# Kernel optimization log

Measured on AMD Instinct MI355X. Metric: run time of the kernel, lower is better.

The kernel has to match this reference:

```python
import jax, jax.numpy as jnp
import numpy as np

B, C, H, W = 16, 64, 128, 128
E = 8          # number of experts
TOPK = 2       # num_expert (top-k routing)


def setup_inputs() -> dict:
    key = jax.random.key(0)
    ks = jax.random.split(key, 8)
    s = 1.0 / np.sqrt(C)
    x = jax.random.normal(ks[0], (B, C, H, W), dtype=jnp.float32)
    k = jax.random.normal(ks[1], (B, C, 1, 1), dtype=jnp.float32)
    Wg = jax.random.normal(ks[2], (C, E), dtype=jnp.float32) * s
    bg = jnp.zeros((E,), dtype=jnp.float32)
    W1 = jax.random.normal(ks[3], (E, C, C), dtype=jnp.float32) * s  # [E, out, in]
    b1 = jnp.zeros((E, C), dtype=jnp.float32)
    W2 = jax.random.normal(ks[4], (E, C, C), dtype=jnp.float32) * s
    b2 = jnp.zeros((E, C), dtype=jnp.float32)
    return {"x": x, "k": k, "Wg": Wg, "bg": bg, "W1": W1, "b1": b1, "W2": W2, "b2": b2}


def reference(x, k, Wg, bg, W1, b1, W2, b2):
    # --- gate: global avg pool + linear -> [B, E] logits ---
    pooled = x.mean(axis=(2, 3))                              # [B, C]
    logits = pooled @ Wg + bg                                  # [B, E]
    # softmax in fp32 then cast back (matches F.softmax(dtype=torch.float).to(x.dtype))
    weights = jax.nn.softmax(logits.astype(jnp.float32), axis=1).astype(x.dtype)
    topk_w, topk_idx = jax.lax.top_k(weights, TOPK)           # [B, TOPK]
    # scatter top-k weights into dense per-expert mask [B, E]
    mask = jnp.zeros_like(weights).at[jnp.arange(B)[:, None], topk_idx].set(topk_w)
    # --- training branch: run ALL experts, combine with mask ---
    # expert_e(x, k) = W2_e @ gelu((W1_e @ x + b1_e) * k) + b2_e   (1x1 convs)
    h = jnp.einsum('eoc,bchw->ebohw', W1, x) + b1[:, None, :, None, None]
    h = jax.nn.gelu(h * k[None])                               # [E, B, C, H, W]
    y = jnp.einsum('eoc,ebchw->ebohw', W2, h) + b2[:, None, :, None, None]
    out = x + jnp.einsum('ebchw,be->bchw', y, mask)
    return out
```

## Files before the change

### kernel.cpp

```cpp
#include <hip/hip_runtime.h>
#include <hip/hip_bf16.h>


#define BB 16
#define CC 64
#define EE 8
#define HWPX 16384
#define LSTR 40

typedef __bf16 bf16x8 __attribute__((ext_vector_type(8)));
typedef float f32x4 __attribute__((ext_vector_type(4)));

__device__ __forceinline__ unsigned packbf2(float lo, float hi) {
    __bf16 a = (__bf16)lo, b = (__bf16)hi;
    unsigned short ua = __builtin_bit_cast(unsigned short, a);
    unsigned short ub = __builtin_bit_cast(unsigned short, b);
    return ((unsigned)ub << 16) | (unsigned)ua;
}

__global__ __launch_bounds__(256) void pool_conv_kernel(
    const float* __restrict__ x, float* __restrict__ pooled,
    const float* __restrict__ W1, const float* __restrict__ W2,
    __bf16* __restrict__ W1b, __bf16* __restrict__ W2b) {
    int blk = blockIdx.x;
    if (blk < BB * CC) {
        const float4* p = (const float4*)(x + (size_t)blk * HWPX);
        float s = 0.f;
        for (int i = threadIdx.x; i < HWPX / 4; i += 256) {
            float4 v = p[i];
            s += (v.x + v.y) + (v.z + v.w);
        }
        #pragma unroll
        for (int off = 32; off > 0; off >>= 1) s += __shfl_down(s, off);
        __shared__ float ls[4];
        if ((threadIdx.x & 63) == 0) ls[threadIdx.x >> 6] = s;
        __syncthreads();
        if (threadIdx.x == 0) pooled[blk] = ((ls[0] + ls[1]) + (ls[2] + ls[3])) * (1.0f / (float)HWPX);
    } else {
        int i = (blk - BB * CC) * 256 + threadIdx.x;
        W1b[i] = (__bf16)W1[i];
        W2b[i] = (__bf16)W2[i];
    }
}

__global__ void gate_kernel(const float* __restrict__ pooled,
                            const float* __restrict__ Wg,
                            const float* __restrict__ bg,
                            int* __restrict__ gidx, float* __restrict__ gw) {
    int b = threadIdx.x;
    if (b >= BB) return;
    float logits[EE];
    #pragma unroll
    for (int e = 0; e < EE; ++e) logits[e] = bg[e];
    for (int c = 0; c < CC; ++c) {
        float pv = pooled[b * CC + c];
        #pragma unroll
        for (int e = 0; e < EE; ++e) logits[e] = fmaf(pv, Wg[c * EE + e], logits[e]);
    }
    float m = logits[0];
    #pragma unroll
    for (int e = 1; e < EE; ++e) m = fmaxf(m, logits[e]);
    float w[EE]; float den = 0.f;
    #pragma unroll
    for (int e = 0; e < EE; ++e) { w[e] = expf(logits[e] - m); den += w[e]; }
    float inv = 1.0f / den;
    #pragma unroll
    for (int e = 0; e < EE; ++e) w[e] *= inv;
    int i0 = 0;
    #pragma unroll
    for (int e = 1; e < EE; ++e) if (w[e] > w[i0]) i0 = e;
    int i1 = -1;
    #pragma unroll
    for (int e = 0; e < EE; ++e) {
        if (e == i0) continue;
        if (i1 < 0 || w[e] > w[i1]) i1 = e;
    }
    gidx[b * 2 + 0] = i0; gidx[b * 2 + 1] = i1;
    gw[b * 2 + 0] = w[i0]; gw[b * 2 + 1] = w[i1];
}

__global__ __launch_bounds__(256) void moe_main(
    const float* __restrict__ x, const float* __restrict__ kvec,
    const __bf16* __restrict__ W1b, const float* __restrict__ b1,
    const __bf16* __restrict__ W2b, const float* __restrict__ b2,
    const int* __restrict__ gidx, const float* __restrict__ gw,
    float* __restrict__ out) {

    __shared__ unsigned int xT32[64 * LSTR];
    __shared__ unsigned int hT32[2][64 * LSTR];

    const int blk = blockIdx.x;
    const int b = blk >> 8;
    const int p0 = (blk & 255) << 6;
    const int t = threadIdx.x;
    const int w = t >> 6;
    const int l = t & 63;
    const int g = l >> 4;
    const int l15 = l & 15;

    const int arow = 16 * w + l15;
    const int r0w = 16 * w + 4 * g;

    const int e0 = __builtin_amdgcn_readfirstlane(gidx[b * 2 + 0]);
    const int e1 = __builtin_amdgcn_readfirstlane(gidx[b * 2 + 1]);
    const float wgt0 = gw[b * 2 + 0];
    const float wgt1 = gw[b * 2 + 1];

    bf16x8 a1f[2][2], a2f[2][2];
    #pragma unroll
    for (int ks = 0; ks < 2; ++ks) {
        a1f[0][ks] = *(const bf16x8*)(W1b + e0 * CC * CC + arow * CC + ks * 32 + g * 8);
        a1f[1][ks] = *(const bf16x8*)(W1b + e1 * CC * CC + arow * CC + ks * 32 + g * 8);
        a2f[0][ks] = *(const bf16x8*)(W2b + e0 * CC * CC + arow * CC + ks * 32 + g * 8);
        a2f[1][ks] = *(const bf16x8*)(W2b + e1 * CC * CC + arow * CC + ks * 32 + g * 8);
    }
    float b1j[2][4], b2j[2][4], kkj[4];
    #pragma unroll
    for (int j = 0; j < 4; ++j) {
        b1j[0][j] = b1[e0 * CC + r0w + j];
        b1j[1][j] = b1[e1 * CC + r0w + j];
        b2j[0][j] = b2[e0 * CC + r0w + j];
        b2j[1][j] = b2[e1 * CC + r0w + j];
        kkj[j]    = kvec[b * CC + r0w + j];
    }

    {
        const int c0 = (t & 31) * 2;
        const int px0 = (t >> 5) * 8;
        const float* r0 = x + ((size_t)(b * CC + c0)) * HWPX + p0 + px0;
        const float* r1 = r0 + HWPX;
        float4 A0 = *(const float4*)(r0);
        float4 A1 = *(const float4*)(r0 + 4);
        float4 B0 = *(const float4*)(r1);
        float4 B1 = *(const float4*)(r1 + 4);
        float av[8] = {A0.x, A0.y, A0.z, A0.w, A1.x, A1.y, A1.z, A1.w};
        float bv[8] = {B0.x, B0.y, B0.z, B0.w, B1.x, B1.y, B1.z, B1.w};
        #pragma unroll
        for (int i = 0; i < 8; ++i)
            xT32[(px0 + i) * LSTR + (t & 31)] = packbf2(av[i], bv[i]);
    }
    __syncthreads();

    bf16x8 bx[4][2];
    #pragma unroll
    for (int cb = 0; cb < 4; ++cb)
        #pragma unroll
        for (int ks = 0; ks < 2; ++ks)
            bx[cb][ks] = *(const bf16x8*)&xT32[(cb * 16 + l15) * LSTR + ks * 16 + g * 4];

    f32x4 acc2[4];
    #pragma unroll
    for (int cb = 0; cb < 4; ++cb) acc2[cb] = (f32x4){0.f, 0.f, 0.f, 0.f};

    const float C1 = -2.302208239f;
    const float C2 = -0.1029434f;

    #pragma unroll
    for (int s = 0; s < 2; ++s) {
        const float wgt = s ? wgt1 : wgt0;

        f32x4 hacc[4];
        #pragma unroll
        for (int cb = 0; cb < 4; ++cb) {
            hacc[cb] = (f32x4){0.f, 0.f, 0.f, 0.f};
            #pragma unroll
            for (int ks = 0; ks < 2; ++ks)
                hacc[cb] = __builtin_amdgcn_mfma_f32_16x16x32_bf16(a1f[s][ks], bx[cb][ks], hacc[cb], 0, 0, 0);
        }

        #pragma unroll
        for (int cb = 0; cb < 4; ++cb) {
            float hv[4];
            #pragma unroll
            for (int j = 0; j < 4; ++j) {
                float a = hacc[cb][j] + b1j[s][j];
                float tt = a * kkj[j];
                float tt2 = tt * tt;
                float arg = tt * fmaf(C2, tt2, C1);
                float ex = __builtin_amdgcn_exp2f(arg);
                float r = __builtin_amdgcn_rcpf(ex + 1.f);
                hv[j] = (tt * wgt) * r;
            }
            const int px = cb * 16 + l15;
            uint2 pk;
            pk.x = packbf2(hv[0], hv[1]);
            pk.y = packbf2(hv[2], hv[3]);
            *(uint2*)&hT32[s][px * LSTR + 8 * w + 2 * g] = pk;
        }
        __syncthreads();

        #pragma unroll
        for (int cb = 0; cb < 4; ++cb) {
            #pragma unroll
            for (int ks = 0; ks < 2; ++ks) {
                bf16x8 bh = *(const bf16x8*)&hT32[s][(cb * 16 + l15) * LSTR + ks * 16 + g * 4];
                acc2[cb] = __builtin_amdgcn_mfma_f32_16x16x32_bf16(a2f[s][ks], bh, acc2[cb], 0, 0, 0);
            }
        }

        #pragma unroll
        for (int j = 0; j < 4; ++j) {
            float bb = wgt * b2j[s][j];
            #pragma unroll
            for (int cb = 0; cb < 4; ++cb) acc2[cb][j] += bb;
        }
    }

    const float* xbase = x + (size_t)b * CC * HWPX + p0;
    float* obase = out + (size_t)b * CC * HWPX + p0;
    #pragma unroll
    for (int cb = 0; cb < 4; ++cb) {
        const int col = cb * 16 + l15;
        #pragma unroll
        for (int j = 0; j < 4; ++j) {
            size_t off = (size_t)(r0w + j) * HWPX + col;
            __builtin_nontemporal_store(xbase[off] + acc2[cb][j], &obase[off]);
        }
    }
}

extern "C" void kernel_launch(void* const* d_in, const int* in_sizes, int n_in,
                              void* d_out, int out_size, void* d_ws, size_t ws_size,
                              hipStream_t stream) {
    const float* x  = (const float*)d_in[0];
    const float* k  = (const float*)d_in[1];
    const float* Wg = (const float*)d_in[2];
    const float* bg = (const float*)d_in[3];
    const float* W1 = (const float*)d_in[4];
    const float* b1 = (const float*)d_in[5];
    const float* W2 = (const float*)d_in[6];
    const float* b2 = (const float*)d_in[7];
    float* out = (float*)d_out;

    float*  pooled = (float*)d_ws;
    int*    gidx   = (int*)((char*)d_ws + 4096);
    float*  gw     = (float*)((char*)d_ws + 4096 + 128);
    __bf16* W1b    = (__bf16*)((char*)d_ws + 8192);
    __bf16* W2b    = (__bf16*)((char*)d_ws + 8192 + 65536);

    pool_conv_kernel<<<BB * CC + EE * CC * CC / 256, 256, 0, stream>>>(x, pooled, W1, W2, W1b, W2b);
    gate_kernel<<<1, 64, 0, stream>>>(pooled, Wg, bg, gidx, gw);
    moe_main<<<BB * 256, 256, 0, stream>>>(x, k, W1b, b1, W2b, b2, gidx, gw, out);
}
```

Baseline: 57.33 us.

## Restructure MoE main kernel: swizzled LDS reuse, interleaved expert GEMMs, early residual loads

Replaces the padded LDS layout with an XOR-swizzled 32-word stride and reuses the x buffer for the second expert's hidden tile, cutting LDS footprint from three buffers to two. Both experts' first GEMMs and GELUs are interleaved for more ILP. W2 fragment loads and residual x loads are deferred and issued ahead of the second GEMM to overlap with LDS work. The bias terms are folded into one combined sum, and the output uses normal rather than nontemporal stores. The interleaving and early loads raise register pressure.

Result: no change. 56.57 us (-1.3%).

```diff
diff --git a/kernel.cpp b/kernel.cpp
--- a/kernel.cpp
+++ b/kernel.cpp
@@ -6,7 +6,6 @@
 #define CC 64
 #define EE 8
 #define HWPX 16384
-#define LSTR 40
 
 typedef __bf16 bf16x8 __attribute__((ext_vector_type(8)));
 typedef float f32x4 __attribute__((ext_vector_type(4)));
@@ -16,6 +15,10 @@
     unsigned short ua = __builtin_bit_cast(unsigned short, a);
     unsigned short ub = __builtin_bit_cast(unsigned short, b);
     return ((unsigned)ub << 16) | (unsigned)ua;
+}
+
+__device__ __forceinline__ int swz(int px, int d) {
+    return px * 32 + ((d & ~3) ^ ((px & 7) << 2)) + (d & 3);
 }
 
 __global__ __launch_bounds__(256) void pool_conv_kernel(
@@ -86,8 +89,7 @@
     const int* __restrict__ gidx, const float* __restrict__ gw,
     float* __restrict__ out) {
 
-    __shared__ unsigned int xT32[64 * LSTR];
-    __shared__ unsigned int hT32[2][64 * LSTR];
+    __shared__ unsigned int lds[2][64 * 32];
 
     const int blk = blockIdx.x;
     const int b = blk >> 8;
@@ -106,13 +108,11 @@
     const float wgt0 = gw[b * 2 + 0];
     const float wgt1 = gw[b * 2 + 1];
 
-    bf16x8 a1f[2][2], a2f[2][2];
+    bf16x8 a1f[2][2];
     #pragma unroll
     for (int ks = 0; ks < 2; ++ks) {
         a1f[0][ks] = *(const bf16x8*)(W1b + e0 * CC * CC + arow * CC + ks * 32 + g * 8);
         a1f[1][ks] = *(const bf16x8*)(W1b + e1 * CC * CC + arow * CC + ks * 32 + g * 8);
-        a2f[0][ks] = *(const bf16x8*)(W2b + e0 * CC * CC + arow * CC + ks * 32 + g * 8);
-        a2f[1][ks] = *(const bf16x8*)(W2b + e1 * CC * CC + arow * CC + ks * 32 + g * 8);
     }
     float b1j[2][4], b2j[2][4], kkj[4];
     #pragma unroll
@@ -125,9 +125,9 @@
     }
 
     {
-        const int c0 = (t & 31) * 2;
+        const int c0 = (t & 31);
         const int px0 = (t >> 5) * 8;
-        const float* r0 = x + ((size_t)(b * CC + c0)) * HWPX + p0 + px0;
+        const float* r0 = x + ((size_t)(b * CC + c0 * 2)) * HWPX + p0 + px0;
         const float* r1 = r0 + HWPX;
         float4 A0 = *(const float4*)(r0);
         float4 A1 = *(const float4*)(r0 + 4);
@@ -137,7 +137,7 @@
         float bv[8] = {B0.x, B0.y, B0.z, B0.w, B1.x, B1.y, B1.z, B1.w};
         #pragma unroll
         for (int i = 0; i < 8; ++i)
-            xT32[(px0 + i) * LSTR + (t & 31)] = packbf2(av[i], bv[i]);
+            lds[0][swz(px0 + i, c0)] = packbf2(av[i], bv[i]);
     }
     __syncthreads();
 
@@ -146,67 +146,98 @@
     for (int cb = 0; cb < 4; ++cb)
         #pragma unroll
         for (int ks = 0; ks < 2; ++ks)
-            bx[cb][ks] = *(const bf16x8*)&xT32[(cb * 16 + l15) * LSTR + ks * 16 + g * 4];
-
-    f32x4 acc2[4];
-    #pragma unroll
-    for (int cb = 0; cb < 4; ++cb) acc2[cb] = (f32x4){0.f, 0.f, 0.f, 0.f};
+            bx[cb][ks] = *(const bf16x8*)&lds[0][swz(cb * 16 + l15, ks * 16 + g * 4)];
 
     const float C1 = -2.302208239f;
     const float C2 = -0.1029434f;
 
-    #pragma unroll
-    for (int s = 0; s < 2; ++s) {
-        const float wgt = s ? wgt1 : wgt0;
-
-        f32x4 hacc[4];
-        #pragma unroll
-        for (int cb = 0; cb < 4; ++cb) {
-            hacc[cb] = (f32x4){0.f, 0.f, 0.f, 0.f};
-            #pragma unroll
-            for (int ks = 0; ks < 2; ++ks)
-                hacc[cb] = __builtin_amdgcn_mfma_f32_16x16x32_bf16(a1f[s][ks], bx[cb][ks], hacc[cb], 0, 0, 0);
-        }
-
-        #pragma unroll
-        for (int cb = 0; cb < 4; ++cb) {
-            float hv[4];
-            #pragma unroll
-            for (int j = 0; j < 4; ++j) {
-                float a = hacc[cb][j] + b1j[s][j];
-                float tt = a * kkj[j];
-                float tt2 = tt * tt;
-                float arg = tt * fmaf(C2, tt2, C1);
-                float ex = __builtin_amdgcn_exp2f(arg);
-                float r = __builtin_amdgcn_rcpf(ex + 1.f);
-                hv[j] = (tt * wgt) * r;
-            }
-            const int px = cb * 16 + l15;
-            uint2 pk;
-            pk.x = packbf2(hv[0], hv[1]);
-            pk.y = packbf2(hv[2], hv[3]);
-            *(uint2*)&hT32[s][px * LSTR + 8 * w + 2 * g] = pk;
-        }
-        __syncthreads();
-
-        #pragma unroll
-        for (int cb = 0; cb < 4; ++cb) {
-            #pragma unroll
-            for (int ks = 0; ks < 2; ++ks) {
-                bf16x8 bh = *(const bf16x8*)&hT32[s][(cb * 16 + l15) * LSTR + ks * 16 + g * 4];
-                acc2[cb] = __builtin_amdgcn_mfma_f32_16x16x32_bf16(a2f[s][ks], bh, acc2[cb], 0, 0, 0);
-            }
-        }
-
+    f32x4 h0[4], h1[4];
+    #pragma unroll
+    for (int cb = 0; cb < 4; ++cb) {
+        h0[cb] = (f32x4){0.f, 0.f, 0.f, 0.f};
+        h1[cb] = (f32x4){0.f, 0.f, 0.f, 0.f};
+        #pragma unroll
+        for (int ks = 0; ks < 2; ++ks) {
+            h0[cb] = __builtin_amdgcn_mfma_f32_16x16x32_bf16(a1f[0][ks], bx[cb][ks], h0[cb], 0, 0, 0);
+            h1[cb] = __builtin_amdgcn_mfma_f32_16x16x32_bf16(a1f[1][ks], bx[cb][ks], h1[cb], 0, 0, 0);
+        }
+    }
+
+    uint2 p0k[4], p1k[4];
+    #pragma unroll
+    for (int cb = 0; cb < 4; ++cb) {
+        float hv0[4], hv1[4];
         #pragma unroll
         for (int j = 0; j < 4; ++j) {
-            float bb = wgt * b2j[s][j];
-            #pragma unroll
-            for (int cb = 0; cb < 4; ++cb) acc2[cb][j] += bb;
-        }
-    }
+            float a0 = h0[cb][j] + b1j[0][j];
+            float t0 = a0 * kkj[j];
+            float ex0 = __builtin_amdgcn_exp2f(t0 * fmaf(C2, t0 * t0, C1));
+            hv0[j] = (t0 * wgt0) * __builtin_amdgcn_rcpf(ex0 + 1.f);
+            float a1 = h1[cb][j] + b1j[1][j];
+            float t1 = a1 * kkj[j];
+            float ex1 = __builtin_amdgcn_exp2f(t1 * fmaf(C2, t1 * t1, C1));
+            hv1[j] = (t1 * wgt1) * __builtin_amdgcn_rcpf(ex1 + 1.f);
+        }
+        p0k[cb].x = packbf2(hv0[0], hv0[1]);
+        p0k[cb].y = packbf2(hv0[2], hv0[3]);
+        p1k[cb].x = packbf2(hv1[0], hv1[1]);
+        p1k[cb].y = packbf2(hv1[2], hv1[3]);
+    }
+
+    #pragma unroll
+    for (int cb = 0; cb < 4; ++cb)
+        *(uint2*)&lds[1][swz(cb * 16 + l15, 8 * w + 2 * g)] = p0k[cb];
+
+    bf16x8 a2f[2][2];
+    #pragma unroll
+    for (int ks = 0; ks < 2; ++ks) {
+        a2f[0][ks] = *(const bf16x8*)(W2b + e0 * CC * CC + arow * CC + ks * 32 + g * 8);
+        a2f[1][ks] = *(const bf16x8*)(W2b + e1 * CC * CC + arow * CC + ks * 32 + g * 8);
+    }
+
+    __syncthreads();
+
+    #pragma unroll
+    for (int cb = 0; cb < 4; ++cb)
+        *(uint2*)&lds[0][swz(cb * 16 + l15, 8 * w + 2 * g)] = p1k[cb];
 
     const float* xbase = x + (size_t)b * CC * HWPX + p0;
+    float xp[4][4];
+    #pragma unroll
+    for (int cb = 0; cb < 4; ++cb)
+        #pragma unroll
+        for (int j = 0; j < 4; ++j)
+            xp[cb][j] = xbase[(size_t)(r0w + j) * HWPX + cb * 16 + l15];
+
+    f32x4 acc2[4];
+    #pragma unroll
+    for (int cb = 0; cb < 4; ++cb) acc2[cb] = (f32x4){0.f, 0.f, 0.f, 0.f};
+
+    #pragma unroll
+    for (int cb = 0; cb < 4; ++cb) {
+        #pragma unroll
+        for (int ks = 0; ks < 2; ++ks) {
+            bf16x8 bh = *(const bf16x8*)&lds[1][swz(cb * 16 + l15, ks * 16 + g * 4)];
+            acc2[cb] = __builtin_amdgcn_mfma_f32_16x16x32_bf16(a2f[0][ks], bh, acc2[cb], 0, 0, 0);
+        }
+    }
+
+    __syncthreads();
+
+    #pragma unroll
+    for (int cb = 0; cb < 4; ++cb) {
+        #pragma unroll
+        for (int ks = 0; ks < 2; ++ks) {
+            bf16x8 bh = *(const bf16x8*)&lds[0][swz(cb * 16 + l15, ks * 16 + g * 4)];
+            acc2[cb] = __builtin_amdgcn_mfma_f32_16x16x32_bf16(a2f[1][ks], bh, acc2[cb], 0, 0, 0);
+        }
+    }
+
+    float bsum[4];
+    #pragma unroll
+    for (int j = 0; j < 4; ++j)
+        bsum[j] = fmaf(wgt0, b2j[0][j], wgt1 * b2j[1][j]);
+
     float* obase = out + (size_t)b * CC * HWPX + p0;
     #pragma unroll
     for (int cb = 0; cb < 4; ++cb) {
@@ -214,7 +245,7 @@
         #pragma unroll
         for (int j = 0; j < 4; ++j) {
             size_t off = (size_t)(r0w + j) * HWPX + col;
-            __builtin_nontemporal_store(xbase[off] + acc2[cb][j], &obase[off]);
+            obase[off] = xp[cb][j] + (acc2[cb][j] + bsum[j]);
         }
     }
 }
```

## Give each wave its own pixel tile so x is reused from registers

Applied to the files above, without the earlier changes.

Each wave now owns 16 pixels and computes all 64 output channels across four row tiles, instead of the block sharing a transposed x tile and splitting channels across waves. The x values are loaded once into registers and reused for the residual add, which removes the second global read of x. Per-wave swizzled LDS buffers replace the block-wide padded buffers and __syncthreads barriers. The b2 bias terms are pre-combined. In exchange, every wave now loads the full weight matrices, which adds register pressure under the launch_bounds(256,4) hint, and x loads are only 16 pixels wide per channel row and uses plain rather than nontemporal stores.

Result: slower. 95.80 us (+67.1%).

```diff
diff --git a/kernel.cpp b/kernel.cpp
--- a/kernel.cpp
+++ b/kernel.cpp
@@ -6,7 +6,6 @@
 #define CC 64
 #define EE 8
 #define HWPX 16384
-#define LSTR 40
 
 typedef __bf16 bf16x8 __attribute__((ext_vector_type(8)));
 typedef float f32x4 __attribute__((ext_vector_type(4)));
@@ -16,6 +15,10 @@
     unsigned short ua = __builtin_bit_cast(unsigned short, a);
     unsigned short ub = __builtin_bit_cast(unsigned short, b);
     return ((unsigned)ub << 16) | (unsigned)ua;
+}
+
+__device__ __forceinline__ int swz16(int p, int d) {
+    return p * 32 + ((d & ~3) ^ ((p & 7) << 2)) + (d & 3);
 }
 
 __global__ __launch_bounds__(256) void pool_conv_kernel(
@@ -79,144 +82,160 @@
     gw[b * 2 + 0] = w[i0]; gw[b * 2 + 1] = w[i1];
 }
 
-__global__ __launch_bounds__(256) void moe_main(
+__global__ __launch_bounds__(256, 4) void moe_main(
     const float* __restrict__ x, const float* __restrict__ kvec,
     const __bf16* __restrict__ W1b, const float* __restrict__ b1,
     const __bf16* __restrict__ W2b, const float* __restrict__ b2,
     const int* __restrict__ gidx, const float* __restrict__ gw,
     float* __restrict__ out) {
 
-    __shared__ unsigned int xT32[64 * LSTR];
-    __shared__ unsigned int hT32[2][64 * LSTR];
+    __shared__ unsigned int LH[4][2][16 * 32];
 
     const int blk = blockIdx.x;
     const int b = blk >> 8;
-    const int p0 = (blk & 255) << 6;
+    const int P0 = (blk & 255) << 6;
     const int t = threadIdx.x;
     const int w = t >> 6;
     const int l = t & 63;
     const int g = l >> 4;
     const int l15 = l & 15;
-
-    const int arow = 16 * w + l15;
-    const int r0w = 16 * w + 4 * g;
+    const int px = P0 + 16 * w + l15;
 
     const int e0 = __builtin_amdgcn_readfirstlane(gidx[b * 2 + 0]);
     const int e1 = __builtin_amdgcn_readfirstlane(gidx[b * 2 + 1]);
     const float wgt0 = gw[b * 2 + 0];
     const float wgt1 = gw[b * 2 + 1];
 
-    bf16x8 a1f[2][2], a2f[2][2];
-    #pragma unroll
-    for (int ks = 0; ks < 2; ++ks) {
-        a1f[0][ks] = *(const bf16x8*)(W1b + e0 * CC * CC + arow * CC + ks * 32 + g * 8);
-        a1f[1][ks] = *(const bf16x8*)(W1b + e1 * CC * CC + arow * CC + ks * 32 + g * 8);
-        a2f[0][ks] = *(const bf16x8*)(W2b + e0 * CC * CC + arow * CC + ks * 32 + g * 8);
-        a2f[1][ks] = *(const bf16x8*)(W2b + e1 * CC * CC + arow * CC + ks * 32 + g * 8);
-    }
-    float b1j[2][4], b2j[2][4], kkj[4];
-    #pragma unroll
-    for (int j = 0; j < 4; ++j) {
-        b1j[0][j] = b1[e0 * CC + r0w + j];
-        b1j[1][j] = b1[e1 * CC + r0w + j];
-        b2j[0][j] = b2[e0 * CC + r0w + j];
-        b2j[1][j] = b2[e1 * CC + r0w + j];
-        kkj[j]    = kvec[b * CC + r0w + j];
-    }
-
-    {
-        const int c0 = (t & 31) * 2;
-        const int px0 = (t >> 5) * 8;
-        const float* r0 = x + ((size_t)(b * CC + c0)) * HWPX + p0 + px0;
-        const float* r1 = r0 + HWPX;
-        float4 A0 = *(const float4*)(r0);
-        float4 A1 = *(const float4*)(r0 + 4);
-        float4 B0 = *(const float4*)(r1);
-        float4 B1 = *(const float4*)(r1 + 4);
-        float av[8] = {A0.x, A0.y, A0.z, A0.w, A1.x, A1.y, A1.z, A1.w};
-        float bv[8] = {B0.x, B0.y, B0.z, B0.w, B1.x, B1.y, B1.z, B1.w};
-        #pragma unroll
-        for (int i = 0; i < 8; ++i)
-            xT32[(px0 + i) * LSTR + (t & 31)] = packbf2(av[i], bv[i]);
-    }
-    __syncthreads();
-
-    bf16x8 bx[4][2];
-    #pragma unroll
-    for (int cb = 0; cb < 4; ++cb)
-        #pragma unroll
-        for (int ks = 0; ks < 2; ++ks)
-            bx[cb][ks] = *(const bf16x8*)&xT32[(cb * 16 + l15) * LSTR + ks * 16 + g * 4];
-
-    f32x4 acc2[4];
-    #pragma unroll
-    for (int cb = 0; cb < 4; ++cb) acc2[cb] = (f32x4){0.f, 0.f, 0.f, 0.f};
+    const float* xb = x + b * CC * HWPX + px;
+    unsigned int* L0 = &LH[w][0][0];
+    unsigned int* L1 = &LH[w][1][0];
+
+    float xc[16];
+    #pragma unroll
+    for (int rt = 0; rt < 4; ++rt)
+        #pragma unroll
+        for (int j = 0; j < 4; ++j)
+            xc[rt * 4 + j] = xb[(rt * 16 + 4 * g + j) * HWPX];
+
+    #pragma unroll
+    for (int rt = 0; rt < 4; ++rt) {
+        uint2 pk;
+        pk.x = packbf2(xc[rt * 4 + 0], xc[rt * 4 + 1]);
+        pk.y = packbf2(xc[rt * 4 + 2], xc[rt * 4 + 3]);
+        *(uint2*)&L0[swz16(l15, rt * 8 + 2 * g)] = pk;
+    }
+    bf16x8 bx0 = *(const bf16x8*)&L0[swz16(l15, 4 * g)];
+    bf16x8 bx1 = *(const bf16x8*)&L0[swz16(l15, 16 + 4 * g)];
+
+    f32x4 b1v0[4], b1v1[4], kk[4], bsum[4];
+    #pragma unroll
+    for (int rt = 0; rt < 4; ++rt) {
+        b1v0[rt] = *(const f32x4*)(b1 + e0 * CC + rt * 16 + 4 * g);
+        b1v1[rt] = *(const f32x4*)(b1 + e1 * CC + rt * 16 + 4 * g);
+        f32x4 b2v0 = *(const f32x4*)(b2 + e0 * CC + rt * 16 + 4 * g);
+        f32x4 b2v1 = *(const f32x4*)(b2 + e1 * CC + rt * 16 + 4 * g);
+        kk[rt] = *(const f32x4*)(kvec + b * CC + rt * 16 + 4 * g);
+        #pragma unroll
+        for (int j = 0; j < 4; ++j) bsum[rt][j] = fmaf(wgt0, b2v0[j], wgt1 * b2v1[j]);
+    }
 
     const float C1 = -2.302208239f;
     const float C2 = -0.1029434f;
 
-    #pragma unroll
-    for (int s = 0; s < 2; ++s) {
-        const float wgt = s ? wgt1 : wgt0;
-
-        f32x4 hacc[4];
-        #pragma unroll
-        for (int cb = 0; cb < 4; ++cb) {
-            hacc[cb] = (f32x4){0.f, 0.f, 0.f, 0.f};
-            #pragma unroll
-            for (int ks = 0; ks < 2; ++ks)
-                hacc[cb] = __builtin_amdgcn_mfma_f32_16x16x32_bf16(a1f[s][ks], bx[cb][ks], hacc[cb], 0, 0, 0);
-        }
-
-        #pragma unroll
-        for (int cb = 0; cb < 4; ++cb) {
+    bf16x8 a[4][2];
+
+    {
+        const __bf16* W1e = W1b + e0 * CC * CC;
+        #pragma unroll
+        for (int rt = 0; rt < 4; ++rt) {
+            a[rt][0] = *(const bf16x8*)(W1e + (rt * 16 + l15) * CC + g * 8);
+            a[rt][1] = *(const bf16x8*)(W1e + (rt * 16 + l15) * CC + 32 + g * 8);
+        }
+        #pragma unroll
+        for (int rt = 0; rt < 4; ++rt) {
+            f32x4 acc = (f32x4){0.f, 0.f, 0.f, 0.f};
+            acc = __builtin_amdgcn_mfma_f32_16x16x32_bf16(a[rt][0], bx0, acc, 0, 0, 0);
+            acc = __builtin_amdgcn_mfma_f32_16x16x32_bf16(a[rt][1], bx1, acc, 0, 0, 0);
             float hv[4];
             #pragma unroll
             for (int j = 0; j < 4; ++j) {
-                float a = hacc[cb][j] + b1j[s][j];
-                float tt = a * kkj[j];
-                float tt2 = tt * tt;
-                float arg = tt * fmaf(C2, tt2, C1);
-                float ex = __builtin_amdgcn_exp2f(arg);
-                float r = __builtin_amdgcn_rcpf(ex + 1.f);
-                hv[j] = (tt * wgt) * r;
+                float tt = (acc[j] + b1v0[rt][j]) * kk[rt][j];
+                float ex = __builtin_amdgcn_exp2f(tt * fmaf(C2, tt * tt, C1));
+                hv[j] = (tt * wgt0) * __builtin_amdgcn_rcpf(ex + 1.f);
             }
-            const int px = cb * 16 + l15;
             uint2 pk;
             pk.x = packbf2(hv[0], hv[1]);
             pk.y = packbf2(hv[2], hv[3]);
-            *(uint2*)&hT32[s][px * LSTR + 8 * w + 2 * g] = pk;
-        }
-        __syncthreads();
-
-        #pragma unroll
-        for (int cb = 0; cb < 4; ++cb) {
+            *(uint2*)&L0[swz16(l15, rt * 8 + 2 * g)] = pk;
+        }
+    }
+
+    {
+        const __bf16* W1e = W1b + e1 * CC * CC;
+        #pragma unroll
+        for (int rt = 0; rt < 4; ++rt) {
+            a[rt][0] = *(const bf16x8*)(W1e + (rt * 16 + l15) * CC + g * 8);
+            a[rt][1] = *(const bf16x8*)(W1e + (rt * 16 + l15) * CC + 32 + g * 8);
+        }
+        #pragma unroll
+        for (int rt = 0; rt < 4; ++rt) {
+            f32x4 acc = (f32x4){0.f, 0.f, 0.f, 0.f};
+            acc = __builtin_amdgcn_mfma_f32_16x16x32_bf16(a[rt][0], bx0, acc, 0, 0, 0);
+            acc = __builtin_amdgcn_mfma_f32_16x16x32_bf16(a[rt][1], bx1, acc, 0, 0, 0);
+            float hv[4];
             #pragma unroll
-            for (int ks = 0; ks < 2; ++ks) {
-                bf16x8 bh = *(const bf16x8*)&hT32[s][(cb * 16 + l15) * LSTR + ks * 16 + g * 4];
-                acc2[cb] = __builtin_amdgcn_mfma_f32_16x16x32_bf16(a2f[s][ks], bh, acc2[cb], 0, 0, 0);
+            for (int j = 0; j < 4; ++j) {
+                float tt = (acc[j] + b1v1[rt][j]) * kk[rt][j];
+                float ex = __builtin_amdgcn_exp2f(tt * fmaf(C2, tt * tt, C1));
+                hv[j] = (tt * wgt1) * __builtin_amdgcn_rcpf(ex + 1.f);
             }
-        }
-
-        #pragma unroll
-        for (int j = 0; j < 4; ++j) {
-            float bb = wgt * b2j[s][j];
-            #pragma unroll
-            for (int cb = 0; cb < 4; ++cb) acc2[cb][j] += bb;
-        }
-    }
-
-    const float* xbase = x + (size_t)b * CC * HWPX + p0;
-    float* obase = out + (size_t)b * CC * HWPX + p0;
-    #pragma unroll
-    for (int cb = 0; cb < 4; ++cb) {
-        const int col = cb * 16 + l15;
-        #pragma unroll
-        for (int j = 0; j < 4; ++j) {
-            size_t off = (size_t)(r0w + j) * HWPX + col;
-            __builtin_nontemporal_store(xbase[off] + acc2[cb][j], &obase[off]);
-        }
-    }
+            uint2 pk;
+            pk.x = packbf2(hv[0], hv[1]);
+            pk.y = packbf2(hv[2], hv[3]);
+            *(uint2*)&L1[swz16(l15, rt * 8 + 2 * g)] = pk;
+        }
+    }
+
+    bf16x8 bh00 = *(const bf16x8*)&L0[swz16(l15, 4 * g)];
+    bf16x8 bh01 = *(const bf16x8*)&L0[swz16(l15, 16 + 4 * g)];
+    bf16x8 bh10 = *(const bf16x8*)&L1[swz16(l15, 4 * g)];
+    bf16x8 bh11 = *(const bf16x8*)&L1[swz16(l15, 16 + 4 * g)];
+
+    f32x4 acc2[4];
+    {
+        const __bf16* W2e = W2b + e0 * CC * CC;
+        #pragma unroll
+        for (int rt = 0; rt < 4; ++rt) {
+            a[rt][0] = *(const bf16x8*)(W2e + (rt * 16 + l15) * CC + g * 8);
+            a[rt][1] = *(const bf16x8*)(W2e + (rt * 16 + l15) * CC + 32 + g * 8);
+        }
+        #pragma unroll
+        for (int rt = 0; rt < 4; ++rt) {
+            acc2[rt] = (f32x4){0.f, 0.f, 0.f, 0.f};
+            acc2[rt] = __builtin_amdgcn_mfma_f32_16x16x32_bf16(a[rt][0], bh00, acc2[rt], 0, 0, 0);
+            acc2[rt] = __builtin_amdgcn_mfma_f32_16x16x32_bf16(a[rt][1], bh01, acc2[rt], 0, 0, 0);
+        }
+    }
+    {
+        const __bf16* W2e = W2b + e1 * CC * CC;
+        #pragma unroll
+        for (int rt = 0; rt < 4; ++rt) {
+            a[rt][0] = *(const bf16x8*)(W2e + (rt * 16 + l15) * CC + g * 8);
+            a[rt][1] = *(const bf16x8*)(W2e + (rt * 16 + l15) * CC + 32 + g * 8);
+        }
+        #pragma unroll
+        for (int rt = 0; rt < 4; ++rt) {
+            acc2[rt] = __builtin_amdgcn_mfma_f32_16x16x32_bf16(a[rt][0], bh10, acc2[rt], 0, 0, 0);
+            acc2[rt] = __builtin_amdgcn_mfma_f32_16x16x32_bf16(a[rt][1], bh11, acc2[rt], 0, 0, 0);
+        }
+    }
+
+    float* ob = out + b * CC * HWPX + px;
+    #pragma unroll
+    for (int rt = 0; rt < 4; ++rt)
+        #pragma unroll
+        for (int j = 0; j < 4; ++j)
+            ob[(rt * 16 + 4 * g + j) * HWPX] = xc[rt * 4 + j] + (acc2[rt][j] + bsum[rt][j]);
 }
 
 extern "C" void kernel_launch(void* const* d_in, const int* in_sizes, int n_in,
```
